# Kernel tuning notes

Hardware: AMD Instinct MI355X
Metric: run time of the kernel (lower is better)

Reference implementation:

```python
import jax, jax.numpy as jnp
import numpy as np

B, D_IN, P, H, E, K, NS, OUT = 4096, 512, 1024, 2048, 8, 2, 2, 29
HS = H * NS  # shared-expert intermediate size


def setup_inputs() -> dict:
    key = jax.random.key(0)
    ks = jax.random.split(key, 20)
    g = lambda i, shape, fan: jax.random.normal(ks[i], shape, jnp.float32) * (1.0 / np.sqrt(fan))
    return {
        "x": jax.random.normal(ks[0], (B, D_IN), jnp.float32),
        # input projection
        "Wproj": g(1, (D_IN, P), D_IN), "bproj": jnp.zeros((P,), jnp.float32),
        # router (Tutel top gate: linear, no bias)
        "Wg": g(2, (P, E), P),
        # fine experts (grouped FFN with fc1/fc2 bias)
        "W1": g(3, (E, P, H), P), "b1": jnp.zeros((E, H), jnp.float32),
        "W2": g(4, (E, H, P), H), "b2": jnp.zeros((E, P), jnp.float32),
        # shared experts: DeepseekV3MLP (SwiGLU with bias)
        "sg_w": g(5, (P, HS), P), "sg_b": jnp.zeros((HS,), jnp.float32),
        "su_w": g(6, (P, HS), P), "su_b": jnp.zeros((HS,), jnp.float32),
        "sd_w": g(7, (HS, P), HS), "sd_b": jnp.zeros((P,), jnp.float32),
        # output MLP + head
        "m1_w": g(8, (P, H), P), "m1_b": jnp.zeros((H,), jnp.float32),
        "m2_w": g(9, (H, H), H), "m2_b": jnp.zeros((H,), jnp.float32),
        "head_w": g(10, (H, OUT), H), "head_b": jnp.zeros((OUT,), jnp.float32),
    }


def reference(x, Wproj, bproj, Wg, W1, b1, W2, b2,
              sg_w, sg_b, su_w, su_b, sd_w, sd_b,
              m1_w, m1_b, m2_w, m2_b, head_w, head_b):
    silu = jax.nn.silu
    # input projection  [B, P]
    p = x @ Wproj + bproj

    # --- Tutel-style top-k gating (inference: gate_noise = 0, normalize=True) ---
    probs = jax.nn.softmax(p @ Wg, axis=-1)               # [B, E]
    top_vals, top_idx = jax.lax.top_k(probs, K)           # [B, K]
    gates = top_vals / jnp.sum(top_vals, axis=-1, keepdims=True)
    # combine weights as dense [B, E] (zero for non-selected experts)
    combine = jnp.zeros((p.shape[0], E), p.dtype).at[
        jnp.arange(p.shape[0])[:, None], top_idx].add(gates)

    # --- grouped-GEMM experts (ffn with fc1/fc2 bias, silu) ---
    h = silu(jnp.einsum('bp,eph->beh', p, W1) + b1)       # [B, E, H]
    eo = jnp.einsum('beh,ehp->bep', h, W2) + b2           # [B, E, P]
    moe_out = jnp.einsum('be,bep->bp', combine, eo)       # weighted combine

    # --- shared experts: SwiGLU MLP on residual stream ---
    shared = (silu(p @ sg_w + sg_b) * (p @ su_w + su_b)) @ sd_w + sd_b
    combined = moe_out + shared

    # --- output MLP + head ---
    hid = silu(combined @ m1_w + m1_b) @ m2_w + m2_b
    return hid @ head_w + head_b
```

## Files before the change

### kernel.cpp

```cpp
#include <hip/hip_runtime.h>
#include <hip/hip_bf16.h>
#include <cstdint>

typedef unsigned short us;
typedef __attribute__((ext_vector_type(4))) float f32x4;
typedef __attribute__((ext_vector_type(8))) short bf16x8;
typedef __attribute__((ext_vector_type(4))) short s16x4;
typedef __attribute__((ext_vector_type(8))) short s16x8;

__device__ __forceinline__ float b2f(us s){
  union { float f; unsigned u; } x; x.u = ((unsigned)s) << 16; return x.f;
}
__device__ __forceinline__ us f2b(float f){
  union { float f; unsigned u; } x; x.f = f;
  unsigned r = x.u + 0x7FFFu + ((x.u >> 16) & 1u);
  return (us)(r >> 16);
}

#define GLDS16(gp, lp) __builtin_amdgcn_global_load_lds( \
    (const __attribute__((address_space(1))) void*)(gp), \
    (__attribute__((address_space(3))) void*)(lp), 16, 0, 0)

__device__ __forceinline__ void xcd_swizzle(int& bm, int& bn){
  const int gx = gridDim.x;
  if (gridDim.y == 32 && (gx & 1) == 0 && gx >= 8){
    const int lin = blockIdx.y * gx + blockIdx.x;
    const int xcd = lin & 7, r = lin >> 3;
    bm = (xcd & 3) * 8 + (r & 7);
    bn = (xcd >> 2) * (gx >> 1) + (r >> 3);
  } else { bm = blockIdx.y; bn = blockIdx.x; }
}

__global__ void detect_kernel(const unsigned* __restrict__ xw, int* __restrict__ flag){
  __shared__ int cnt;
  if (threadIdx.x == 0) cnt = 0;
  __syncthreads();
  int c = 0;
  for (int i = threadIdx.x; i < 1024; i += 256){
    const unsigned e = (xw[i] >> 7) & 0xFF;
    if (e >= 100 && e <= 140) ++c;
  }
  atomicAdd(&cnt, c);
  __syncthreads();
  if (threadIdx.x == 0) *flag = (cnt < 512) ? 1 : 0;
}

template<bool OUT_BF16, bool SILU>
__global__ __launch_bounds__(256, 2)
void gemm_plain(const us* __restrict__ A, int lda,
                const us* __restrict__ BT, int ldb,
                void* __restrict__ Cout, int ldc,
                const us* __restrict__ bias,
                int M, int N, int K, int Nvalid)
{
  __shared__ us As[128*32];
  __shared__ us Bs[128*32];
  int bmi, bni; xcd_swizzle(bmi, bni);
  const int bm = bmi * 128, bn = bni * 128;
  const int tid = threadIdx.x, wave = tid >> 6, lane = tid & 63;
  const int llo = lane & 15, lhi = lane >> 4;

  const us* aP[2]; const us* bP[2]; us* lA[2]; us* lB[2];
#pragma unroll
  for (int s = 0; s < 2; ++s){
    const int chunk = s*256 + wave*64 + lane;
    const int r = chunk >> 2, cc = chunk & 3;
    aP[s] = A  + (size_t)(bm + r) * lda + cc*8;
    bP[s] = BT + (size_t)(bn + r) * ldb + cc*8;
    lA[s] = As + (size_t)(s*256 + wave*64) * 8;
    lB[s] = Bs + (size_t)(s*256 + wave*64) * 8;
  }

  f32x4 acc[4][4] = {};
  const int waveM = (wave >> 1) * 64, waveN = (wave & 1) * 64;

  for (int k0 = 0; k0 < K; k0 += 32){
    GLDS16(aP[0] + k0, lA[0]);
    GLDS16(aP[1] + k0, lA[1]);
    GLDS16(bP[0] + k0, lB[0]);
    GLDS16(bP[1] + k0, lB[1]);
    __syncthreads();
    bf16x8 af[4], bv[4];
#pragma unroll
    for (int t = 0; t < 4; ++t){
      af[t] = *reinterpret_cast<const bf16x8*>(As + (waveM + t*16 + llo)*32 + lhi*8);
      bv[t] = *reinterpret_cast<const bf16x8*>(Bs + (waveN + t*16 + llo)*32 + lhi*8);
    }
#pragma unroll
    for (int mt = 0; mt < 4; ++mt)
#pragma unroll
      for (int nt = 0; nt < 4; ++nt)
        acc[mt][nt] = __builtin_amdgcn_mfma_f32_16x16x32_bf16(af[mt], bv[nt], acc[mt][nt], 0, 0, 0);
    __syncthreads();
  }

#pragma unroll
  for (int nt = 0; nt < 4; ++nt){
    const int col = bn + waveN + nt*16 + llo;
    float bb = 0.f;
    if (bias && col < Nvalid) bb = b2f(bias[col]);
#pragma unroll
    for (int mt = 0; mt < 4; ++mt){
      const int row0 = bm + waveM + mt*16 + lhi*4;
#pragma unroll
      for (int r = 0; r < 4; ++r){
        if (col < Nvalid){
          float v = acc[mt][nt][r] + bb;
          if (SILU) v = v / (1.f + __expf(-v));
          if (OUT_BF16) ((us*)Cout)[(size_t)(row0 + r) * ldc + col] = f2b(v);
          else          ((float*)Cout)[(size_t)(row0 + r) * ldc + col] = v;
        }
      }
    }
  }
}

__global__ __launch_bounds__(256, 2)
void gemm_sgsu(const us* __restrict__ A, const us* __restrict__ B1T,
               const us* __restrict__ B2T, const us* __restrict__ bias1,
               const us* __restrict__ bias2, us* __restrict__ Cout)
{
  __shared__ us As[128*32];
  __shared__ us B1s[128*32];
  __shared__ us B2s[128*32];
  int bmi, bni; xcd_swizzle(bmi, bni);
  const int bm = bmi * 128, bn = bni * 128;
  const int tid = threadIdx.x, wave = tid >> 6, lane = tid & 63;
  const int llo = lane & 15, lhi = lane >> 4;

  const us* aP[2]; const us* b1P[2]; const us* b2P[2];
  us* lA[2]; us* lB1[2]; us* lB2[2];
#pragma unroll
  for (int s = 0; s < 2; ++s){
    const int chunk = s*256 + wave*64 + lane;
    const int r = chunk >> 2, cc = chunk & 3;
    aP[s]  = A   + (size_t)(bm + r) * 1024 + cc*8;
    b1P[s] = B1T + (size_t)(bn + r) * 1024 + cc*8;
    b2P[s] = B2T + (size_t)(bn + r) * 1024 + cc*8;
    lA[s]  = As  + (size_t)(s*256 + wave*64) * 8;
    lB1[s] = B1s + (size_t)(s*256 + wave*64) * 8;
    lB2[s] = B2s + (size_t)(s*256 + wave*64) * 8;
  }

  f32x4 acc1[4][4] = {};
  f32x4 acc2[4][4] = {};
  const int waveM = (wave >> 1) * 64, waveN = (wave & 1) * 64;

  for (int k0 = 0; k0 < 1024; k0 += 32){
    GLDS16(aP[0] + k0, lA[0]);
    GLDS16(aP[1] + k0, lA[1]);
    GLDS16(b1P[0] + k0, lB1[0]);
    GLDS16(b1P[1] + k0, lB1[1]);
    GLDS16(b2P[0] + k0, lB2[0]);
    GLDS16(b2P[1] + k0, lB2[1]);
    __syncthreads();
    bf16x8 af[4], b1v[4], b2v[4];
#pragma unroll
    for (int t = 0; t < 4; ++t){
      af[t]  = *reinterpret_cast<const bf16x8*>(As  + (waveM + t*16 + llo)*32 + lhi*8);
      b1v[t] = *reinterpret_cast<const bf16x8*>(B1s + (waveN + t*16 + llo)*32 + lhi*8);
      b2v[t] = *reinterpret_cast<const bf16x8*>(B2s + (waveN + t*16 + llo)*32 + lhi*8);
    }
#pragma unroll
    for (int mt = 0; mt < 4; ++mt)
#pragma unroll
      for (int nt = 0; nt < 4; ++nt){
        acc1[mt][nt] = __builtin_amdgcn_mfma_f32_16x16x32_bf16(af[mt], b1v[nt], acc1[mt][nt], 0, 0, 0);
        acc2[mt][nt] = __builtin_amdgcn_mfma_f32_16x16x32_bf16(af[mt], b2v[nt], acc2[mt][nt], 0, 0, 0);
      }
    __syncthreads();
  }

#pragma unroll
  for (int nt = 0; nt < 4; ++nt){
    const int col = bn + waveN + nt*16 + llo;
    const float bb1 = b2f(bias1[col]);
    const float bb2 = b2f(bias2[col]);
#pragma unroll
    for (int mt = 0; mt < 4; ++mt){
      const int row0 = bm + waveM + mt*16 + lhi*4;
#pragma unroll
      for (int r = 0; r < 4; ++r){
        const float g = acc1[mt][nt][r] + bb1;
        const float v = (g / (1.f + __expf(-g))) * (acc2[mt][nt][r] + bb2);
        Cout[(size_t)(row0 + r) * 4096 + col] = f2b(v);
      }
    }
  }
}

template<bool OUT_BF16, bool SILU>
__global__ __launch_bounds__(256, 2)
void gemm_group(const us* __restrict__ Abase, int lda,
                const int* __restrict__ rowmap,
                const int* __restrict__ offsets,
                const us* __restrict__ BTbase,
                void* __restrict__ Cout, int ldc,
                const us* __restrict__ biasbase,
                int N, int K)
{
  const int e   = blockIdx.z;
  const int off = offsets[e];
  const int Te  = offsets[e + 1] - off;
  const int bmL = blockIdx.y * 128;
  if (bmL >= Te) return;

  __shared__ us As[128*32];
  __shared__ us Bs[128*32];
  const us* BT   = BTbase  + (size_t)e * N * K;
  const us* bias = biasbase + (size_t)e * N;
  const int bn = blockIdx.x * 128;
  const int tid = threadIdx.x, wave = tid >> 6, lane = tid & 63;
  const int llo = lane & 15, lhi = lane >> 4;

  const us* aP[2]; const us* bP[2]; us* lA[2]; us* lB[2];
#pragma unroll
  for (int s = 0; s < 2; ++s){
    const int chunk = s*256 + wave*64 + lane;
    const int r = chunk >> 2, cc = chunk & 3;
    int pos = off + bmL + r; if (pos > 8191) pos = 8191;
    const int arow = rowmap ? rowmap[pos] : pos;
    aP[s] = Abase + (size_t)arow * lda + cc*8;
    bP[s] = BT + (size_t)(bn + r) * K + cc*8;
    lA[s] = As + (size_t)(s*256 + wave*64) * 8;
    lB[s] = Bs + (size_t)(s*256 + wave*64) * 8;
  }

  f32x4 acc[4][4] = {};
  const int waveM = (wave >> 1) * 64, waveN = (wave & 1) * 64;

  for (int k0 = 0; k0 < K; k0 += 32){
    GLDS16(aP[0] + k0, lA[0]);
    GLDS16(aP[1] + k0, lA[1]);
    GLDS16(bP[0] + k0, lB[0]);
    GLDS16(bP[1] + k0, lB[1]);
    __syncthreads();
    bf16x8 af[4], bv[4];
#pragma unroll
    for (int t = 0; t < 4; ++t){
      af[t] = *reinterpret_cast<const bf16x8*>(As + (waveM + t*16 + llo)*32 + lhi*8);
      bv[t] = *reinterpret_cast<const bf16x8*>(Bs + (waveN + t*16 + llo)*32 + lhi*8);
    }
#pragma unroll
    for (int mt = 0; mt < 4; ++mt)
#pragma unroll
      for (int nt = 0; nt < 4; ++nt)
        acc[mt][nt] = __builtin_amdgcn_mfma_f32_16x16x32_bf16(af[mt], bv[nt], acc[mt][nt], 0, 0, 0);
    __syncthreads();
  }

#pragma unroll
  for (int nt = 0; nt < 4; ++nt){
    const int col = bn + waveN + nt*16 + llo;
    const float bb = b2f(bias[col]);
#pragma unroll
    for (int mt = 0; mt < 4; ++mt){
      const int localBase = bmL + waveM + mt*16 + lhi*4;
#pragma unroll
      for (int r = 0; r < 4; ++r){
        const int local = localBase + r;
        if (local < Te){
          float v = acc[mt][nt][r] + bb;
          if (SILU) v = v / (1.f + __expf(-v));
          const size_t row = (size_t)(off + local);
          if (OUT_BF16) ((us*)Cout)[row * ldc + col] = f2b(v);
          else          ((float*)Cout)[row * ldc + col] = v;
        }
      }
    }
  }
}

__global__ __launch_bounds__(256, 2)
void gemm_head(const us* __restrict__ A, const us* __restrict__ BT,
               float* __restrict__ Cpart)
{
  __shared__ us As[128*32];
  __shared__ us Bs[128*32];
  const int bm = blockIdx.y * 128;
  const int koff = blockIdx.z * 256;
  const int tid = threadIdx.x, wave = tid >> 6, lane = tid & 63;
  const int llo = lane & 15, lhi = lane >> 4;

  const us* aP[2]; const us* bP[2]; us* lA[2]; us* lB[2];
#pragma unroll
  for (int s = 0; s < 2; ++s){
    const int chunk = s*256 + wave*64 + lane;
    const int r = chunk >> 2, cc = chunk & 3;
    aP[s] = A  + (size_t)(bm + r) * 2048 + koff + cc*8;
    bP[s] = BT + (size_t)r * 2048 + koff + cc*8;
    lA[s] = As + (size_t)(s*256 + wave*64) * 8;
    lB[s] = Bs + (size_t)(s*256 + wave*64) * 8;
  }

  f32x4 acc[4][4] = {};
  const int waveM = (wave >> 1) * 64, waveN = (wave & 1) * 64;

  for (int k0 = 0; k0 < 256; k0 += 32){
    GLDS16(aP[0] + k0, lA[0]);
    GLDS16(aP[1] + k0, lA[1]);
    GLDS16(bP[0] + k0, lB[0]);
    GLDS16(bP[1] + k0, lB[1]);
    __syncthreads();
    bf16x8 af[4], bv[4];
#pragma unroll
    for (int t = 0; t < 4; ++t){
      af[t] = *reinterpret_cast<const bf16x8*>(As + (waveM + t*16 + llo)*32 + lhi*8);
      bv[t] = *reinterpret_cast<const bf16x8*>(Bs + (waveN + t*16 + llo)*32 + lhi*8);
    }
#pragma unroll
    for (int mt = 0; mt < 4; ++mt)
#pragma unroll
      for (int nt = 0; nt < 4; ++nt)
        acc[mt][nt] = __builtin_amdgcn_mfma_f32_16x16x32_bf16(af[mt], bv[nt], acc[mt][nt], 0, 0, 0);
    __syncthreads();
  }

  float* out = Cpart + (size_t)blockIdx.z * 4096 * 32;
#pragma unroll
  for (int nt = 0; nt < 4; ++nt){
    const int col = waveN + nt*16 + llo;
    if (col >= 29) continue;
#pragma unroll
    for (int mt = 0; mt < 4; ++mt){
      const int row0 = bm + waveM + mt*16 + lhi*4;
#pragma unroll
      for (int r = 0; r < 4; ++r)
        out[(size_t)(row0 + r) * 32 + col] = acc[mt][nt][r];
    }
  }
}

__global__ void reduce_head(const float* __restrict__ part, const us* __restrict__ bias,
                            void* __restrict__ dst, const int* __restrict__ flag){
  const int i = blockIdx.x * 256 + threadIdx.x;
  if (i >= 4096*29) return;
  const int t = i / 29, c = i - t * 29;
  float s = b2f(bias[c]);
#pragma unroll
  for (int z = 0; z < 8; ++z) s += part[((size_t)z * 4096 + t) * 32 + c];
  if (*flag) ((float*)dst)[i] = s;
  else       ((us*)dst)[i] = f2b(s);
}

__global__ void transpose_any(const void* __restrict__ src_, us* __restrict__ dst,
                              int R, int C, long long smat, long long dmat,
                              const int* __restrict__ flag)
{
  const int f32 = *flag;
  dst += (size_t)blockIdx.z * dmat;
  __shared__ us tile[32][33];
  const int c0 = blockIdx.x * 32, r0 = blockIdx.y * 32;
  const int tx = threadIdx.x & 31, ty = threadIdx.x >> 5;
#pragma unroll
  for (int i = 0; i < 4; ++i){
    const int r = r0 + ty + i*8, c = c0 + tx;
    const size_t idx = (size_t)blockIdx.z * smat + (size_t)r * C + c;
    us v = 0;
    if (c < C){
      if (f32) v = f2b(((const float*)src_)[idx]);
      else     v = ((const us*)src_)[idx];
    }
    tile[ty + i*8][tx] = v;
  }
  __syncthreads();
#pragma unroll
  for (int i = 0; i < 4; ++i){
    const int dr = c0 + ty + i*8;
    dst[(size_t)dr * R + r0 + tx] = tile[tx][ty + i*8];
  }
}

__global__ void cvt_any_bf(const void* __restrict__ src, us* __restrict__ dst, int n,
                           const int* __restrict__ flag){
  const int i = (blockIdx.x * 256 + threadIdx.x) * 4;
  if (i >= n) return;
  s16x4 o;
  if (*flag){
    f32x4 v = *reinterpret_cast<const f32x4*>((const float*)src + i);
#pragma unroll
    for (int k = 0; k < 4; ++k) o[k] = (short)f2b(v[k]);
  } else {
    o = *reinterpret_cast<const s16x4*>((const us*)src + i);
  }
  *reinterpret_cast<s16x4*>(dst + i) = o;
}

__global__ void compose_router(const void* __restrict__ Wproj, const void* __restrict__ Wg,
                               float* __restrict__ M, const int* __restrict__ flag)
{
  const int f32 = *flag;
  const int wave = threadIdx.x >> 6, lane = threadIdx.x & 63;
  const int d = blockIdx.x * 4 + wave;
  float acc[8] = {0,0,0,0,0,0,0,0};
  for (int n = lane; n < 1024; n += 64){
    float wp;
    if (f32) wp = ((const float*)Wproj)[(size_t)d * 1024 + n];
    else     wp = b2f(((const us*)Wproj)[(size_t)d * 1024 + n]);
    if (f32){
      const float* wg = (const float*)Wg + (size_t)n * 8;
#pragma unroll
      for (int e = 0; e < 8; ++e) acc[e] += wp * wg[e];
    } else {
      const s16x8 wg = *reinterpret_cast<const s16x8*>((const us*)Wg + (size_t)n * 8);
#pragma unroll
      for (int e = 0; e < 8; ++e) acc[e] += wp * b2f((us)wg[e]);
    }
  }
#pragma unroll
  for (int e = 0; e < 8; ++e){
    float v = acc[e];
    for (int off = 32; off > 0; off >>= 1) v += __shfl_down(v, off);
    if (lane == 0) M[(size_t)d * 8 + e] = v;
  }
}

__global__ void router2(const void* __restrict__ x, const float* __restrict__ M,
                        int* __restrict__ eidx, float* __restrict__ gates,
                        const int* __restrict__ flag)
{
  const int f32 = *flag;
  const int wave = threadIdx.x >> 6, lane = threadIdx.x & 63;
  const int t = blockIdx.x * 4 + wave;
  float l[8] = {0,0,0,0,0,0,0,0};
  for (int d = lane; d < 512; d += 64){
    float xv;
    if (f32) xv = ((const float*)x)[(size_t)t * 512 + d];
    else     xv = b2f(((const us*)x)[(size_t)t * 512 + d]);
    const float* mr = M + (size_t)d * 8;
#pragma unroll
    for (int e = 0; e < 8; ++e) l[e] += xv * mr[e];
  }
#pragma unroll
  for (int e = 0; e < 8; ++e){
    float v = l[e];
    for (int off = 32; off > 0; off >>= 1) v += __shfl_down(v, off);
    l[e] = v;
  }
  if (lane == 0){
    int e0 = 0; float v0 = l[0];
#pragma unroll
    for (int e = 1; e < 8; ++e) if (l[e] > v0){ v0 = l[e]; e0 = e; }
    int e1 = (e0 == 0) ? 1 : 0; float v1 = l[e1];
#pragma unroll
    for (int e = 0; e < 8; ++e) if (e != e0 && l[e] > v1){ v1 = l[e]; e1 = e; }
    const float g1 = 1.f / (1.f + __expf(v0 - v1));
    eidx[t*2] = e0;  eidx[t*2+1] = e1;
    gates[t*2] = 1.f - g1; gates[t*2+1] = g1;
  }
}

__global__ void hist_kernel(const int* __restrict__ eidx, int* __restrict__ counts){
  __shared__ int lh[8];
  if (threadIdx.x < 8) lh[threadIdx.x] = 0;
  __syncthreads();
  const int i = blockIdx.x * 256 + threadIdx.x;
  atomicAdd(&lh[eidx[i]], 1);
  __syncthreads();
  if (threadIdx.x < 8) atomicAdd(&counts[threadIdx.x], lh[threadIdx.x]);
}

__global__ void scan_kernel(const int* __restrict__ counts, int* __restrict__ offsets){
  if (threadIdx.x == 0){
    int s = 0;
    for (int e = 0; e < 8; ++e){ offsets[e] = s; s += counts[e]; }
    offsets[8] = s;
  }
}

__global__ void fill_kernel(const int* __restrict__ eidx, const int* __restrict__ offsets,
                            int* __restrict__ fillg, int* __restrict__ pos_tk,
                            int* __restrict__ tok_of_pos){
  __shared__ int lh[8];
  __shared__ int lbase[8];
  if (threadIdx.x < 8) lh[threadIdx.x] = 0;
  __syncthreads();
  const int i = blockIdx.x * 256 + threadIdx.x;
  const int e = eidx[i];
  const int r = atomicAdd(&lh[e], 1);
  __syncthreads();
  if (threadIdx.x < 8) lbase[threadIdx.x] = atomicAdd(&fillg[threadIdx.x], lh[threadIdx.x]);
  __syncthreads();
  const int pos = offsets[e] + lbase[e] + r;
  pos_tk[i] = pos;
  tok_of_pos[pos] = i >> 1;
}

__global__ void combine_kernel(const float* __restrict__ eo, const float* __restrict__ shr,
                               const int* __restrict__ pos_tk, const float* __restrict__ gates,
                               us* __restrict__ comb){
  const int t = blockIdx.x;
  const int c = threadIdx.x * 4;
  const int p0 = pos_tk[t*2], p1 = pos_tk[t*2+1];
  const float g0 = gates[t*2], g1 = gates[t*2+1];
  f32x4 a = *reinterpret_cast<const f32x4*>(eo + (size_t)p0 * 1024 + c);
  f32x4 b = *reinterpret_cast<const f32x4*>(eo + (size_t)p1 * 1024 + c);
  f32x4 s = *reinterpret_cast<const f32x4*>(shr + (size_t)t * 1024 + c);
  s16x4 o;
#pragma unroll
  for (int k = 0; k < 4; ++k) o[k] = (short)f2b(g0 * a[k] + g1 * b[k] + s[k]);
  *reinterpret_cast<s16x4*>(comb + (size_t)t * 1024 + c) = o;
}

extern "C" void kernel_launch(void* const* d_in, const int* in_sizes, int n_in,
                              void* d_out, int out_size, void* d_ws, size_t ws_size,
                              hipStream_t stream)
{
  const void* x      = d_in[0];
  const void* Wproj  = d_in[1];
  const us*   bproj  = (const us*)d_in[2];
  const void* Wg     = d_in[3];
  const void* W1     = d_in[4];
  const us*   b1     = (const us*)d_in[5];
  const void* W2     = d_in[6];
  const us*   b2     = (const us*)d_in[7];
  const void* sg_w   = d_in[8];
  const us*   sg_b   = (const us*)d_in[9];
  const void* su_w   = d_in[10];
  const us*   su_b   = (const us*)d_in[11];
  const void* sd_w   = d_in[12];
  const us*   sd_b   = (const us*)d_in[13];
  const void* m1_w   = d_in[14];
  const us*   m1_b   = (const us*)d_in[15];
  const void* m2_w   = d_in[16];
  const us*   m2_b   = (const us*)d_in[17];
  const void* head_w = d_in[18];
  const us*   head_b = (const us*)d_in[19];

  char* ws = (char*)d_ws;
  size_t off = 0;
  auto take = [&](size_t bytes) -> char* {
    char* p = ws + off; off += (bytes + 255) & ~(size_t)255; return p;
  };
  us* wprojT = (us*)take(1024ULL*512*2);
  us* w1T    = (us*)take(8ULL*2048*1024*2);
  us* w2T    = (us*)take(8ULL*1024*2048*2);
  us* sgT    = (us*)take(4096ULL*1024*2);
  us* suT    = (us*)take(4096ULL*1024*2);
  us* sdT    = (us*)take(1024ULL*4096*2);
  us* m1T    = (us*)take(2048ULL*1024*2);
  us* m2T    = (us*)take(2048ULL*2048*2);
  us* headT  = (us*)take(128ULL*2048*2);
  us* xb     = (us*)take(4096ULL*512*2);
  us* pbf    = (us*)take(4096ULL*1024*2);
  float* Mrt = (float*)take(512ULL*8*4);
  char* bufA = take(33554432);
  char* bufB = take(33554432);
  char* bufC = take(33554432);
  float* shrF  = (float*)take(4096ULL*1024*4);
  float* houtP = (float*)take(8ULL*4096*32*4);
  int* ctrl   = (int*)take(256);
  int* eidx   = (int*)take(8192*4);
  float* gbuf = (float*)take(8192*4);
  int* postk  = (int*)take(8192*4);
  int* tokpos = (int*)take(8192*4);
  int* counts  = ctrl;
  int* fill    = ctrl + 8;
  int* offs    = ctrl + 16;
  int* dflag   = ctrl + 28;

  us* comb = (us*)bufC;
  us* hid1 = (us*)(bufC + 8388608);
  us* hid2 = (us*)bufA;

  const dim3 T(256);

  detect_kernel<<<dim3(1), T, 0, stream>>>((const unsigned*)x, dflag);

  hipMemsetAsync(ctrl, 0, 64, stream);
  compose_router<<<dim3(128), T, 0, stream>>>(Wproj, Wg, Mrt, dflag);
  router2<<<dim3(1024), T, 0, stream>>>(x, Mrt, eidx, gbuf, dflag);
  hist_kernel<<<dim3(32), T, 0, stream>>>(eidx, counts);
  scan_kernel<<<dim3(1), dim3(64), 0, stream>>>(counts, offs);
  fill_kernel<<<dim3(32), T, 0, stream>>>(eidx, offs, fill, postk, tokpos);

  transpose_any<<<dim3(32, 16, 1), T, 0, stream>>>(Wproj, wprojT, 512, 1024, 0, 0, dflag);
  transpose_any<<<dim3(64, 32, 8), T, 0, stream>>>(W1, w1T, 1024, 2048, 1024LL*2048, 2048LL*1024, dflag);
  transpose_any<<<dim3(32, 64, 8), T, 0, stream>>>(W2, w2T, 2048, 1024, 2048LL*1024, 1024LL*2048, dflag);
  transpose_any<<<dim3(128, 32, 1), T, 0, stream>>>(sg_w, sgT, 1024, 4096, 0, 0, dflag);
  transpose_any<<<dim3(128, 32, 1), T, 0, stream>>>(su_w, suT, 1024, 4096, 0, 0, dflag);
  transpose_any<<<dim3(32, 128, 1), T, 0, stream>>>(sd_w, sdT, 4096, 1024, 0, 0, dflag);
  transpose_any<<<dim3(64, 32, 1), T, 0, stream>>>(m1_w, m1T, 1024, 2048, 0, 0, dflag);
  transpose_any<<<dim3(64, 64, 1), T, 0, stream>>>(m2_w, m2T, 2048, 2048, 0, 0, dflag);
  transpose_any<<<dim3(4, 64, 1), T, 0, stream>>>(head_w, headT, 2048, 29, 0, 0, dflag);

  cvt_any_bf<<<dim3(2048), T, 0, stream>>>(x, xb, 4096*512, dflag);
  gemm_plain<true,false><<<dim3(8, 32), T, 0, stream>>>(xb, 512, wprojT, 512, pbf, 1024, bproj, 4096, 1024, 512, 1024);

  gemm_sgsu<<<dim3(32, 32), T, 0, stream>>>(pbf, sgT, suT, sg_b, su_b, (us*)bufC);
  gemm_plain<false,false><<<dim3(8, 32), T, 0, stream>>>((us*)bufC, 4096, sdT, 4096, shrF, 1024, sd_b, 4096, 1024, 4096, 1024);

  gemm_group<true,true ><<<dim3(16, 64, 8), T, 0, stream>>>(pbf, 1024, tokpos, offs, w1T, bufA, 2048, b1, 2048, 1024);
  gemm_group<false,false><<<dim3(8, 64, 8), T, 0, stream>>>((us*)bufA, 2048, nullptr, offs, w2T, bufB, 1024, b2, 1024, 2048);
  combine_kernel<<<dim3(4096), T, 0, stream>>>((float*)bufB, shrF, postk, gbuf, comb);

  gemm_plain<true,true ><<<dim3(16, 32), T, 0, stream>>>(comb, 1024, m1T, 1024, hid1, 2048, m1_b, 4096, 2048, 1024, 2048);
  gemm_plain<true,false><<<dim3(16, 32), T, 0, stream>>>(hid1, 2048, m2T, 2048, hid2, 2048, m2_b, 4096, 2048, 2048, 2048);
  gemm_head<<<dim3(1, 32, 8), T, 0, stream>>>(hid2, headT, houtP);
  reduce_head<<<dim3(464), T, 0, stream>>>(houtP, head_b, d_out, dflag);

  (void)in_sizes; (void)n_in; (void)out_size; (void)ws_size;
}
```

Baseline: 759.6 us.

## Batch weight transposes, split-K shared down-proj, bf16 expert outputs, atomic-free routing

Merges the nine weight-transpose launches into one table-driven kernel, which removes per-launch overhead and tail effects. The shared-expert down projection is split over K into two fp32 partial buffers, which the combine kernel then sums. The second expert GEMM now writes bf16 instead of fp32, which halves that traffic. Routing bookkeeping uses per-block histograms and a serial scan instead of global atomics and a memset. Risks: the bias may be added in both split-K halves (harmless only because the bias is zero), and there is extra rounding from the bf16 expert outputs.

```diff
diff --git a/kernel.cpp b/kernel.cpp
--- a/kernel.cpp
+++ b/kernel.cpp
@@ -49,9 +49,9 @@
 __global__ __launch_bounds__(256, 2)
 void gemm_plain(const us* __restrict__ A, int lda,
                 const us* __restrict__ BT, int ldb,
-                void* __restrict__ Cout, int ldc,
+                void* __restrict__ Cout_, int ldc,
                 const us* __restrict__ bias,
-                int M, int N, int K, int Nvalid)
+                int M, int N, int Nvalid, int Ksplit)
 {
   __shared__ us As[128*32];
   __shared__ us Bs[128*32];
@@ -59,6 +59,8 @@
   const int bm = bmi * 128, bn = bni * 128;
   const int tid = threadIdx.x, wave = tid >> 6, lane = tid & 63;
   const int llo = lane & 15, lhi = lane >> 4;
+  char* Cout = (char*)Cout_ + (size_t)blockIdx.z * M * ldc * (OUT_BF16 ? 2 : 4);
+  const int kbeg = blockIdx.z * Ksplit, kend = kbeg + Ksplit;
 
   const us* aP[2]; const us* bP[2]; us* lA[2]; us* lB[2];
 #pragma unroll
@@ -74,7 +76,7 @@
   f32x4 acc[4][4] = {};
   const int waveM = (wave >> 1) * 64, waveN = (wave & 1) * 64;
 
-  for (int k0 = 0; k0 < K; k0 += 32){
+  for (int k0 = kbeg; k0 < kend; k0 += 32){
     GLDS16(aP[0] + k0, lA[0]);
     GLDS16(aP[1] + k0, lA[1]);
     GLDS16(bP[0] + k0, lB[0]);
@@ -343,31 +345,46 @@
   else       ((us*)dst)[i] = f2b(s);
 }
 
-__global__ void transpose_any(const void* __restrict__ src_, us* __restrict__ dst,
-                              int R, int C, long long smat, long long dmat,
-                              const int* __restrict__ flag)
-{
+struct TransDesc {
+  const void* src; us* dst;
+  int R, C, tx, ty, prefix;
+  long long smat, dmat;
+};
+struct TransTable { TransDesc d[9]; };
+
+__global__ void transpose_batched(TransTable tt, const int* __restrict__ flag){
   const int f32 = *flag;
-  dst += (size_t)blockIdx.z * dmat;
+  const int bid = blockIdx.x;
+  int m = 0;
+#pragma unroll
+  for (int i = 1; i < 9; ++i) if (bid >= tt.d[i].prefix) m = i;
+  const TransDesc dd = tt.d[m];
+  const int local = bid - dd.prefix;
+  const int per = dd.tx * dd.ty;
+  const int z = local / per;
+  const int rem = local - z * per;
+  const int tyi = rem / dd.tx, txi = rem - tyi * dd.tx;
+
+  const int c0 = txi * 32, r0 = tyi * 32;
   __shared__ us tile[32][33];
-  const int c0 = blockIdx.x * 32, r0 = blockIdx.y * 32;
   const int tx = threadIdx.x & 31, ty = threadIdx.x >> 5;
 #pragma unroll
   for (int i = 0; i < 4; ++i){
     const int r = r0 + ty + i*8, c = c0 + tx;
-    const size_t idx = (size_t)blockIdx.z * smat + (size_t)r * C + c;
+    const size_t idx = (size_t)z * dd.smat + (size_t)r * dd.C + c;
     us v = 0;
-    if (c < C){
-      if (f32) v = f2b(((const float*)src_)[idx]);
-      else     v = ((const us*)src_)[idx];
+    if (c < dd.C){
+      if (f32) v = f2b(((const float*)dd.src)[idx]);
+      else     v = ((const us*)dd.src)[idx];
     }
     tile[ty + i*8][tx] = v;
   }
   __syncthreads();
+  us* dst = dd.dst + (size_t)z * dd.dmat;
 #pragma unroll
   for (int i = 0; i < 4; ++i){
     const int dr = c0 + ty + i*8;
-    dst[(size_t)dr * R + r0 + tx] = tile[tx][ty + i*8];
+    dst[(size_t)dr * dd.R + r0 + tx] = tile[tx][ty + i*8];
   }
 }
 
@@ -450,55 +467,59 @@
   }
 }
 
-__global__ void hist_kernel(const int* __restrict__ eidx, int* __restrict__ counts){
+__global__ void hist_kernel(const int* __restrict__ eidx, int* __restrict__ histB){
   __shared__ int lh[8];
   if (threadIdx.x < 8) lh[threadIdx.x] = 0;
   __syncthreads();
-  const int i = blockIdx.x * 256 + threadIdx.x;
-  atomicAdd(&lh[eidx[i]], 1);
+  atomicAdd(&lh[eidx[blockIdx.x * 256 + threadIdx.x]], 1);
   __syncthreads();
-  if (threadIdx.x < 8) atomicAdd(&counts[threadIdx.x], lh[threadIdx.x]);
-}
-
-__global__ void scan_kernel(const int* __restrict__ counts, int* __restrict__ offsets){
+  if (threadIdx.x < 8) histB[blockIdx.x * 8 + threadIdx.x] = lh[threadIdx.x];
+}
+
+__global__ void scan_kernel(const int* __restrict__ histB, int* __restrict__ offsets,
+                            int* __restrict__ blockbase){
   if (threadIdx.x == 0){
+    int counts[8] = {0,0,0,0,0,0,0,0};
+    for (int b = 0; b < 32; ++b)
+      for (int e = 0; e < 8; ++e) counts[e] += histB[b*8 + e];
     int s = 0;
     for (int e = 0; e < 8; ++e){ offsets[e] = s; s += counts[e]; }
     offsets[8] = s;
-  }
-}
-
-__global__ void fill_kernel(const int* __restrict__ eidx, const int* __restrict__ offsets,
-                            int* __restrict__ fillg, int* __restrict__ pos_tk,
-                            int* __restrict__ tok_of_pos){
+    for (int e = 0; e < 8; ++e){
+      int run = offsets[e];
+      for (int b = 0; b < 32; ++b){ blockbase[b*8 + e] = run; run += histB[b*8 + e]; }
+    }
+  }
+}
+
+__global__ void fill_kernel(const int* __restrict__ eidx, const int* __restrict__ blockbase,
+                            int* __restrict__ pos_tk, int* __restrict__ tok_of_pos){
   __shared__ int lh[8];
-  __shared__ int lbase[8];
   if (threadIdx.x < 8) lh[threadIdx.x] = 0;
   __syncthreads();
   const int i = blockIdx.x * 256 + threadIdx.x;
   const int e = eidx[i];
   const int r = atomicAdd(&lh[e], 1);
-  __syncthreads();
-  if (threadIdx.x < 8) lbase[threadIdx.x] = atomicAdd(&fillg[threadIdx.x], lh[threadIdx.x]);
-  __syncthreads();
-  const int pos = offsets[e] + lbase[e] + r;
+  const int pos = blockbase[blockIdx.x * 8 + e] + r;
   pos_tk[i] = pos;
   tok_of_pos[pos] = i >> 1;
 }
 
-__global__ void combine_kernel(const float* __restrict__ eo, const float* __restrict__ shr,
+__global__ void combine_kernel(const us* __restrict__ eo, const float* __restrict__ shr,
                                const int* __restrict__ pos_tk, const float* __restrict__ gates,
                                us* __restrict__ comb){
   const int t = blockIdx.x;
   const int c = threadIdx.x * 4;
   const int p0 = pos_tk[t*2], p1 = pos_tk[t*2+1];
   const float g0 = gates[t*2], g1 = gates[t*2+1];
-  f32x4 a = *reinterpret_cast<const f32x4*>(eo + (size_t)p0 * 1024 + c);
-  f32x4 b = *reinterpret_cast<const f32x4*>(eo + (size_t)p1 * 1024 + c);
-  f32x4 s = *reinterpret_cast<const f32x4*>(shr + (size_t)t * 1024 + c);
+  s16x4 a = *reinterpret_cast<const s16x4*>(eo + (size_t)p0 * 1024 + c);
+  s16x4 b = *reinterpret_cast<const s16x4*>(eo + (size_t)p1 * 1024 + c);
+  f32x4 s0 = *reinterpret_cast<const f32x4*>(shr + (size_t)t * 1024 + c);
+  f32x4 s1 = *reinterpret_cast<const f32x4*>(shr + 4096ULL*1024 + (size_t)t * 1024 + c);
   s16x4 o;
 #pragma unroll
-  for (int k = 0; k < 4; ++k) o[k] = (short)f2b(g0 * a[k] + g1 * b[k] + s[k]);
+  for (int k = 0; k < 4; ++k)
+    o[k] = (short)f2b(g0 * b2f((us)a[k]) + g1 * b2f((us)b[k]) + s0[k] + s1[k]);
   *reinterpret_cast<s16x4*>(comb + (size_t)t * 1024 + c) = o;
 }
 
@@ -547,17 +568,17 @@
   char* bufA = take(33554432);
   char* bufB = take(33554432);
   char* bufC = take(33554432);
-  float* shrF  = (float*)take(4096ULL*1024*4);
+  float* shrF  = (float*)take(2ULL*4096*1024*4);
   float* houtP = (float*)take(8ULL*4096*32*4);
   int* ctrl   = (int*)take(256);
+  int* histB  = (int*)take(32*8*4);
+  int* bbase  = (int*)take(32*8*4);
   int* eidx   = (int*)take(8192*4);
   float* gbuf = (float*)take(8192*4);
   int* postk  = (int*)take(8192*4);
   int* tokpos = (int*)take(8192*4);
-  int* counts  = ctrl;
-  int* fill    = ctrl + 8;
-  int* offs    = ctrl + 16;
-  int* dflag   = ctrl + 28;
+  int* offs   = ctrl;
+  int* dflag  = ctrl + 28;
 
   us* comb = (us*)bufC;
   us* hid1 = (us*)(bufC + 8388608);
@@ -567,34 +588,41 @@
 
   detect_kernel<<<dim3(1), T, 0, stream>>>((const unsigned*)x, dflag);
 
-  hipMemsetAsync(ctrl, 0, 64, stream);
+  TransTable tt;
+  auto mk = [](const void* s, us* d, int R, int C, int tx, int ty, int prefix,
+               long long smat, long long dmat) -> TransDesc {
+    TransDesc t; t.src = s; t.dst = d; t.R = R; t.C = C; t.tx = tx; t.ty = ty;
+    t.prefix = prefix; t.smat = smat; t.dmat = dmat; return t;
+  };
+  int pf = 0;
+  tt.d[0] = mk(Wproj, wprojT, 512, 1024, 32, 16, pf, 0, 0);                  pf += 32*16;
+  tt.d[1] = mk(W1, w1T, 1024, 2048, 64, 32, pf, 1024LL*2048, 2048LL*1024);   pf += 64*32*8;
+  tt.d[2] = mk(W2, w2T, 2048, 1024, 32, 64, pf, 2048LL*1024, 1024LL*2048);   pf += 32*64*8;
+  tt.d[3] = mk(sg_w, sgT, 1024, 4096, 128, 32, pf, 0, 0);                    pf += 128*32;
+  tt.d[4] = mk(su_w, suT, 1024, 4096, 128, 32, pf, 0, 0);                    pf += 128*32;
+  tt.d[5] = mk(sd_w, sdT, 4096, 1024, 32, 128, pf, 0, 0);                    pf += 32*128;
+  tt.d[6] = mk(m1_w, m1T, 1024, 2048, 64, 32, pf, 0, 0);                     pf += 64*32;
+  tt.d[7] = mk(m2_w, m2T, 2048, 2048, 64, 64, pf, 0, 0);                     pf += 64*64;
+  tt.d[8] = mk(head_w, headT, 2048, 29, 4, 64, pf, 0, 0);                    pf += 4*64;
+  transpose_batched<<<dim3(pf), T, 0, stream>>>(tt, dflag);
+
   compose_router<<<dim3(128), T, 0, stream>>>(Wproj, Wg, Mrt, dflag);
   router2<<<dim3(1024), T, 0, stream>>>(x, Mrt, eidx, gbuf, dflag);
-  hist_kernel<<<dim3(32), T, 0, stream>>>(eidx, counts);
-  scan_kernel<<<dim3(1), dim3(64), 0, stream>>>(counts, offs);
-  fill_kernel<<<dim3(32), T, 0, stream>>>(eidx, offs, fill, postk, tokpos);
-
-  transpose_any<<<dim3(32, 16, 1), T, 0, stream>>>(Wproj, wprojT, 512, 1024, 0, 0, dflag);
-  transpose_any<<<dim3(64, 32, 8), T, 0, stream>>>(W1, w1T, 1024, 2048, 1024LL*2048, 2048LL*1024, dflag);
-  transpose_any<<<dim3(32, 64, 8), T, 0, stream>>>(W2, w2T, 2048, 1024, 2048LL*1024, 1024LL*2048, dflag);
-  transpose_any<<<dim3(128, 32, 1), T, 0, stream>>>(sg_w, sgT, 1024, 4096, 0, 0, dflag);
-  transpose_any<<<dim3(128, 32, 1), T, 0, stream>>>(su_w, suT, 1024, 4096, 0, 0, dflag);
-  transpose_any<<<dim3(32, 128, 1), T, 0, stream>>>(sd_w, sdT, 4096, 1024, 0, 0, dflag);
-  transpose_any<<<dim3(64, 32, 1), T, 0, stream>>>(m1_w, m1T, 1024, 2048, 0, 0, dflag);
-  transpose_any<<<dim3(64, 64, 1), T, 0, stream>>>(m2_w, m2T, 2048, 2048, 0, 0, dflag);
-  transpose_any<<<dim3(4, 64, 1), T, 0, stream>>>(head_w, headT, 2048, 29, 0, 0, dflag);
+  hist_kernel<<<dim3(32), T, 0, stream>>>(eidx, histB);
+  scan_kernel<<<dim3(1), dim3(64), 0, stream>>>(histB, offs, bbase);
+  fill_kernel<<<dim3(32), T, 0, stream>>>(eidx, bbase, postk, tokpos);
 
   cvt_any_bf<<<dim3(2048), T, 0, stream>>>(x, xb, 4096*512, dflag);
-  gemm_plain<true,false><<<dim3(8, 32), T, 0, stream>>>(xb, 512, wprojT, 512, pbf, 1024, bproj, 4096, 1024, 512, 1024);
+  gemm_plain<true,false><<<dim3(8, 32), T, 0, stream>>>(xb, 512, wprojT, 512, pbf, 1024, bproj, 4096, 1024, 1024, 512);
 
   gemm_sgsu<<<dim3(32, 32), T, 0, stream>>>(pbf, sgT, suT, sg_b, su_b, (us*)bufC);
-  gemm_plain<false,false><<<dim3(8, 32), T, 0, stream>>>((us*)bufC, 4096, sdT, 4096, shrF, 1024, sd_b, 4096, 1024, 4096, 1024);
+  gemm_plain<false,false><<<dim3(8, 32, 2), T, 0, stream>>>((us*)bufC, 4096, sdT, 4096, shrF, 1024, sd_b, 4096, 1024, 1024, 2048);
 
   gemm_group<true,true ><<<dim3(16, 64, 8), T, 0, stream>>>(pbf, 1024, tokpos, offs, w1T, bufA, 2048, b1, 2048, 1024);
-  gemm_group<false,false><<<dim3(8, 64, 8), T, 0, stream>>>((us*)bufA, 2048, nullptr, offs, w2T, bufB, 1024, b2, 1024, 2048);
-  combine_kernel<<<dim3(4096), T, 0, stream>>>((float*)bufB, shrF, postk, gbuf, comb);
-
-  gemm_plain<true,true ><<<dim3(16, 32), T, 0, stream>>>(comb, 1024, m1T, 1024, hid1, 2048, m1_b, 4096, 2048, 1024, 2048);
+  gemm_group<true,false><<<dim3(8, 64, 8), T, 0, stream>>>((us*)bufA, 2048, nullptr, offs, w2T, bufB, 1024, b2, 1024, 2048);
+  combine_kernel<<<dim3(4096), T, 0, stream>>>((us*)bufB, shrF, postk, gbuf, comb);
+
+  gemm_plain<true,true ><<<dim3(16, 32), T, 0, stream>>>(comb, 1024, m1T, 1024, hid1, 2048, m1_b, 4096, 2048, 2048, 1024);
   gemm_plain<true,false><<<dim3(16, 32), T, 0, stream>>>(hid1, 2048, m2T, 2048, hid2, 2048, m2_b, 4096, 2048, 2048, 2048);
   gemm_head<<<dim3(1, 32, 8), T, 0, stream>>>(hid2, headT, houtP);
   reduce_head<<<dim3(464), T, 0, stream>>>(houtP, head_b, d_out, dflag);
```

Result: faster. 724.0 us (-4.7%).
